# Kernel optimization log

Hardware: AMD Instinct MI355X
Metric: run time of the kernel (lower is better)

Reference implementation:

```python
import jax, jax.numpy as jnp
from jax import lax
import numpy as np

N_TOTAL = 262144
NUM_SAMPLE = 1024
KNN_K = 16
NUM_CLASSES = 13
HIDDEN = 128
EPS = 1e-8


def _sqdist(a, b):
    # (Na,3),(Nb,3) -> (Na,Nb) squared euclidean; same argmin as torch.cdist
    return (jnp.sum(a * a, axis=1)[:, None]
            + jnp.sum(b * b, axis=1)[None, :]
            - 2.0 * a @ b.T)


def _farthest_point_sample(xyz, n_samples):
    # sequential FPS starting from index 0 (deterministic start)
    n = xyz.shape[0]

    def step(carry, _):
        min_d2, last = carry
        d2 = jnp.sum((xyz - xyz[last]) ** 2, axis=-1)
        min_d2 = jnp.minimum(min_d2, d2)
        nxt = jnp.argmax(min_d2).astype(jnp.int32)
        return (min_d2, nxt), nxt

    init = (jnp.full((n,), 1e10, dtype=xyz.dtype), jnp.int32(0))
    _, idxs = lax.scan(step, init, None, length=n_samples - 1)
    return jnp.concatenate([jnp.zeros((1,), jnp.int32), idxs])


def _compute_normals(pts, k):
    # PCA normal per point from its k nearest neighbors (self excluded)
    d2 = _sqdist(pts, pts)                      # (S,S), S=1024 -> small
    _, nbr_idx = lax.top_k(-d2, k + 1)
    nbr = pts[nbr_idx[:, 1:]]                   # (S,k,3)
    centered = nbr - jnp.mean(nbr, axis=1, keepdims=True)
    cov = jnp.einsum('ski,skj->sij', centered, centered) / (k - 1)
    _, eigvecs = jnp.linalg.eigh(cov)           # ascending eigenvalues
    normal = eigvecs[..., 0]                    # smallest-eigval eigenvector
    return normal / (jnp.linalg.norm(normal, axis=-1, keepdims=True) + EPS)


def _forward(gaussian_positions, gaussian_colors, W1, b1, W2, b2, W3, b3):
    sample_idx = _farthest_point_sample(gaussian_positions, NUM_SAMPLE)
    dxyz = gaussian_positions[sample_idx]       # (S,3)
    drgb = gaussian_colors[sample_idx]          # (S,3)
    dnrm = _compute_normals(dxyz, KNN_K)        # (S,3)
    feats = jnp.concatenate([dxyz, drgb, dnrm], axis=1)  # (S,9)

    # pointwise segmentation network (stand-in for PointNet++ get_model)
    h = jax.nn.relu(feats @ W1 + b1)
    h = jax.nn.relu(h @ W2 + b2)
    pred = h @ W3 + b3                          # (S, num_classes)

    feat_down = jax.nn.softmax(pred, axis=1)
    lbl_down = jnp.argmax(pred, axis=1)

    # 1-NN label propagation: streaming-min candidate (memory-bound)
    d2_full = _sqdist(gaussian_positions, dxyz)  # (N, S) ~ 1 GB
    nearest = jnp.argmin(d2_full, axis=1)
    return feat_down[nearest], lbl_down[nearest]


def setup_inputs() -> dict:
    key = jax.random.key(0)
    ks = jax.random.split(key, 8)
    pos = jax.random.normal(ks[0], (N_TOTAL, 3), jnp.float32)
    col = jax.random.uniform(ks[1], (N_TOTAL, 3), jnp.float32)
    W1 = jax.random.normal(ks[2], (9, HIDDEN), jnp.float32) / np.sqrt(9.0)
    b1 = jnp.zeros((HIDDEN,), jnp.float32)
    W2 = jax.random.normal(ks[3], (HIDDEN, HIDDEN), jnp.float32) / np.sqrt(HIDDEN)
    b2 = jnp.zeros((HIDDEN,), jnp.float32)
    W3 = jax.random.normal(ks[4], (HIDDEN, NUM_CLASSES), jnp.float32) / np.sqrt(HIDDEN)
    b3 = jnp.zeros((NUM_CLASSES,), jnp.float32)
    return {"gaussian_positions": pos, "gaussian_colors": col,
            "W1": W1, "b1": b1, "W2": W2, "b2": b2, "W3": W3, "b3": b3}


def reference(gaussian_positions, gaussian_colors, W1, b1, W2, b2, W3, b3):
    return _forward(gaussian_positions, gaussian_colors, W1, b1, W2, b2, W3, b3)
```

## Files before the change

### kernel.cpp

```cpp
#include <hip/hip_runtime.h>
#include <math.h>

#define N_TOTAL    262144
#define NUM_SAMPLE 1024
#define FPS_BLOCKS 64
#define FPS_THREADS 256
#define FPS_PPT (N_TOTAL / (FPS_BLOCKS * FPS_THREADS))
#define M_WAVE 8
#define POOL (FPS_BLOCKS * 4 * M_WAVE)
#define ENT_PER_T (POOL / FPS_THREADS)
#define SEL_CAP 1023

__device__ __forceinline__ float addrn(float a, float b) { return __fadd_rn(a, b); }
__device__ __forceinline__ float subrn(float a, float b) { return __fsub_rn(a, b); }
__device__ __forceinline__ float mulrn(float a, float b) { return __fmul_rn(a, b); }

__device__ __forceinline__ float d2rn(float ax, float ay, float az,
                                      float bx, float by, float bz) {
  float dx = subrn(ax, bx), dy = subrn(ay, by), dz = subrn(az, bz);
  return addrn(addrn(mulrn(dx, dx), mulrn(dy, dy)), mulrn(dz, dz));
}

__device__ __forceinline__ unsigned long long shflxor_u64(unsigned long long v, int mk) {
  return (unsigned long long)__shfl_xor((long long)v, mk, 64);
}

template <int CTRL>
__device__ __forceinline__ int dpp_i(int x) {
  return __builtin_amdgcn_update_dpp(x, x, CTRL, 0xF, 0xF, false);
}
__device__ __forceinline__ float wave_fmax_bcast(float v) {
  v = fmaxf(v, __int_as_float(dpp_i<0x111>(__float_as_int(v))));
  v = fmaxf(v, __int_as_float(dpp_i<0x112>(__float_as_int(v))));
  v = fmaxf(v, __int_as_float(dpp_i<0x114>(__float_as_int(v))));
  v = fmaxf(v, __int_as_float(dpp_i<0x118>(__float_as_int(v))));
  v = fmaxf(v, __int_as_float(dpp_i<0x142>(__float_as_int(v))));
  v = fmaxf(v, __int_as_float(dpp_i<0x143>(__float_as_int(v))));
  return __int_as_float(__builtin_amdgcn_readlane(__float_as_int(v), 63));
}
__device__ __forceinline__ unsigned wave_umax_bcast(unsigned v) {
  unsigned o;
  o = (unsigned)dpp_i<0x111>((int)v); v = (o > v) ? o : v;
  o = (unsigned)dpp_i<0x112>((int)v); v = (o > v) ? o : v;
  o = (unsigned)dpp_i<0x114>((int)v); v = (o > v) ? o : v;
  o = (unsigned)dpp_i<0x118>((int)v); v = (o > v) ? o : v;
  o = (unsigned)dpp_i<0x142>((int)v); v = (o > v) ? o : v;
  o = (unsigned)dpp_i<0x143>((int)v); v = (o > v) ? o : v;
  return (unsigned)__builtin_amdgcn_readlane((int)v, 63);
}

__device__ __forceinline__ float slapy2f(float x, float y) {
  float xa = fabsf(x), ya = fabsf(y);
  float w = fmaxf(xa, ya), z = fminf(xa, ya);
  if (z == 0.f) return w;
  float t = z / w;
  return w * __fsqrt_rn(1.f + t * t);
}

__device__ __forceinline__ void slartgf(float f, float g, float& c, float& s, float& r) {
  if (g == 0.f) { c = 1.f; s = 0.f; r = f; }
  else if (f == 0.f) { c = 0.f; s = (g > 0.f) ? 1.f : -1.f; r = fabsf(g); }
  else {
    float d = __fsqrt_rn(f * f + g * g);
    c = fabsf(f) / d;
    r = (f >= 0.f) ? d : -d;
    s = g / r;
  }
}

__device__ void slaev2f(float a, float b, float c0, float& rt1, float& rt2,
                        float& cs1, float& sn1) {
  float sm = a + c0, df = a - c0;
  float adf = fabsf(df), tb = b + b, ab = fabsf(tb);
  float acmx, acmn;
  if (fabsf(a) > fabsf(c0)) { acmx = a; acmn = c0; } else { acmx = c0; acmn = a; }
  float rt;
  if (adf > ab)      { float t = ab / adf; rt = adf * __fsqrt_rn(1.f + t * t); }
  else if (adf < ab) { float t = adf / ab; rt = ab * __fsqrt_rn(1.f + t * t); }
  else               { rt = ab * __fsqrt_rn(2.f); }
  int sgn1;
  if (sm < 0.f)      { rt1 = 0.5f * (sm - rt); sgn1 = -1; rt2 = (acmx / rt1) * acmn - (b / rt1) * b; }
  else if (sm > 0.f) { rt1 = 0.5f * (sm + rt); sgn1 = 1;  rt2 = (acmx / rt1) * acmn - (b / rt1) * b; }
  else               { rt1 = 0.5f * rt; rt2 = -0.5f * rt; sgn1 = 1; }
  float cs; int sgn2;
  if (df >= 0.f) { cs = df + rt; sgn2 = 1; } else { cs = df - rt; sgn2 = -1; }
  float acs = fabsf(cs);
  if (acs > ab) {
    float ct = -tb / cs;
    sn1 = 1.f / __fsqrt_rn(1.f + ct * ct);
    cs1 = ct * sn1;
  } else {
    if (ab == 0.f) { cs1 = 1.f; sn1 = 0.f; }
    else { float tn = -cs / tb; cs1 = 1.f / __fsqrt_rn(1.f + tn * tn); sn1 = tn * cs1; }
  }
  if (sgn1 == sgn2) { float tn = cs1; cs1 = -sn1; sn1 = tn; }
}

#define D_(i) d[(i)-1]
#define E_(i) e[(i)-1]

__device__ void ssteqr3(float d[3], float e[2], float Z[3][3]) {
  const float eps    = 5.9604645e-08f;
  const float eps2   = 3.5527137e-15f;
  const float safmin = 1.17549435e-38f;
  const float ssfmax = 3.0744573e+18f;
  const float ssfmin = 3.0517578e-05f;
  const int n = 3;
  int jtot = 0, nmaxit = 90;
  int l1 = 1;

  while (true) {
    if (l1 > n) break;
    if (l1 > 1) E_(l1 - 1) = 0.f;
    int m = n;
    for (int mm = l1; mm <= n - 1; ++mm) {
      float tst = fabsf(E_(mm));
      if (tst == 0.f) { m = mm; break; }
      if (tst <= (__fsqrt_rn(fabsf(D_(mm))) * __fsqrt_rn(fabsf(D_(mm + 1)))) * eps) {
        E_(mm) = 0.f; m = mm; break;
      }
    }
    int l = l1, lsv = l, lend = m, lendsv = m;
    l1 = m + 1;
    if (lend == l) continue;

    float anorm = fabsf(D_(lend));
    for (int i2 = l; i2 <= lend - 1; ++i2) {
      anorm = fmaxf(anorm, fabsf(D_(i2)));
      anorm = fmaxf(anorm, fabsf(E_(i2)));
    }
    int iscale = 0;
    if (anorm == 0.f) continue;
    if (anorm > ssfmax) {
      iscale = 1; float mul = ssfmax / anorm;
      for (int i2 = l; i2 <= lend; ++i2) D_(i2) *= mul;
      for (int i2 = l; i2 <= lend - 1; ++i2) E_(i2) *= mul;
    } else if (anorm < ssfmin) {
      iscale = 2; float mul = ssfmin / anorm;
      for (int i2 = l; i2 <= lend; ++i2) D_(i2) *= mul;
      for (int i2 = l; i2 <= lend - 1; ++i2) E_(i2) *= mul;
    }

    if (fabsf(D_(lend)) < fabsf(D_(l))) { int t = l; l = lend; lend = t; }

    if (lend > l) {
      while (true) {
        int m2 = lend;
        if (l != lend) {
          for (int mm = l; mm <= lend - 1; ++mm) {
            float tst = fabsf(E_(mm)); tst = tst * tst;
            if (tst <= (eps2 * fabsf(D_(mm))) * fabsf(D_(mm + 1)) + safmin) { m2 = mm; break; }
          }
        }
        if (m2 < lend) E_(m2) = 0.f;
        float p = D_(l);
        if (m2 == l) { D_(l) = p; l = l + 1; if (l <= lend) continue; break; }
        if (m2 == l + 1) {
          float rt1, rt2, cc, ss;
          slaev2f(D_(l), E_(l), D_(l + 1), rt1, rt2, cc, ss);
          for (int i2 = 0; i2 < 3; ++i2) {
            float tmp = Z[i2][l];
            Z[i2][l]     = cc * tmp - ss * Z[i2][l - 1];
            Z[i2][l - 1] = ss * tmp + cc * Z[i2][l - 1];
          }
          D_(l) = rt1; D_(l + 1) = rt2; E_(l) = 0.f;
          l = l + 2; if (l <= lend) continue; break;
        }
        if (jtot == nmaxit) break;
        ++jtot;
        float g = (D_(l + 1) - p) / (2.f * E_(l));
        float r = slapy2f(g, 1.f);
        float sgn_rg = (g >= 0.f) ? r : -r;
        g = D_(m2) - p + E_(l) / (g + sgn_rg);
        float s = 1.f, c = 1.f;
        p = 0.f;
        float csv[2], ssv[2];
        for (int i2 = m2 - 1; i2 >= l; --i2) {
          float f = s * E_(i2);
          float b = c * E_(i2);
          slartgf(g, f, c, s, r);
          if (i2 != m2 - 1) E_(i2 + 1) = r;
          g = D_(i2 + 1) - p;
          r = (D_(i2) - g) * s + 2.f * c * b;
          p = s * r;
          D_(i2 + 1) = g + p;
          g = c * r - b;
          csv[i2 - l] = c; ssv[i2 - l] = -s;
        }
        for (int j = m2 - 1; j >= l; --j) {
          float ct = csv[j - l], st = ssv[j - l];
          for (int i2 = 0; i2 < 3; ++i2) {
            float tmp = Z[i2][j];
            Z[i2][j]     = ct * tmp - st * Z[i2][j - 1];
            Z[i2][j - 1] = st * tmp + ct * Z[i2][j - 1];
          }
        }
        D_(l) = D_(l) - p;
        E_(l) = g;
      }
    } else {
      while (true) {
        int m2 = lend;
        if (l != lend) {
          for (int mm = l; mm >= lend + 1; --mm) {
            float tst = fabsf(E_(mm - 1)); tst = tst * tst;
            if (tst <= (eps2 * fabsf(D_(mm))) * fabsf(D_(mm - 1)) + safmin) { m2 = mm; break; }
          }
        }
        if (m2 > lend) E_(m2 - 1) = 0.f;
        float p = D_(l);
        if (m2 == l) { D_(l) = p; l = l - 1; if (l >= lend) continue; break; }
        if (m2 == l - 1) {
          float rt1, rt2, cc, ss;
          slaev2f(D_(l - 1), E_(l - 1), D_(l), rt1, rt2, cc, ss);
          for (int i2 = 0; i2 < 3; ++i2) {
            float tmp = Z[i2][l - 1];
            Z[i2][l - 1] = cc * tmp - ss * Z[i2][l - 2];
            Z[i2][l - 2] = ss * tmp + cc * Z[i2][l - 2];
          }
          D_(l - 1) = rt1; D_(l) = rt2; E_(l - 1) = 0.f;
          l = l - 2; if (l >= lend) continue; break;
        }
        if (jtot == nmaxit) break;
        ++jtot;
        float g = (D_(l - 1) - p) / (2.f * E_(l - 1));
        float r = slapy2f(g, 1.f);
        float sgn_rg = (g >= 0.f) ? r : -r;
        g = D_(m2) - p + E_(l - 1) / (g + sgn_rg);
        float s = 1.f, c = 1.f;
        p = 0.f;
        float csv[2], ssv[2];
        for (int i2 = m2; i2 <= l - 1; ++i2) {
          float f = s * E_(i2);
          float b = c * E_(i2);
          slartgf(g, f, c, s, r);
          if (i2 != m2) E_(i2 - 1) = r;
          g = D_(i2) - p;
          r = (D_(i2 + 1) - g) * s + 2.f * c * b;
          p = s * r;
          D_(i2) = g + p;
          g = c * r - b;
          csv[i2 - m2] = c; ssv[i2 - m2] = s;
        }
        for (int j = m2; j <= l - 1; ++j) {
          float ct = csv[j - m2], st = ssv[j - m2];
          for (int i2 = 0; i2 < 3; ++i2) {
            float tmp = Z[i2][j];
            Z[i2][j]     = ct * tmp - st * Z[i2][j - 1];
            Z[i2][j - 1] = st * tmp + ct * Z[i2][j - 1];
          }
        }
        D_(l) = D_(l) - p;
        E_(l - 1) = g;
      }
    }
    if (iscale == 1) {
      float mul = anorm / ssfmax;
      for (int i2 = lsv; i2 <= lendsv; ++i2) D_(i2) *= mul;
      for (int i2 = lsv; i2 <= lendsv - 1; ++i2) E_(i2) *= mul;
    } else if (iscale == 2) {
      float mul = anorm / ssfmin;
      for (int i2 = lsv; i2 <= lendsv; ++i2) D_(i2) *= mul;
      for (int i2 = lsv; i2 <= lendsv - 1; ++i2) E_(i2) *= mul;
    }
  }
  for (int ii = 2; ii <= n; ++ii) {
    int i2 = ii - 1, k = i2;
    float p = D_(i2);
    for (int j = ii; j <= n; ++j) if (D_(j) < p) { k = j; p = D_(j); }
    if (k != i2) {
      D_(k) = D_(i2); D_(i2) = p;
      for (int rr = 0; rr < 3; ++rr) {
        float t = Z[rr][i2 - 1]; Z[rr][i2 - 1] = Z[rr][k - 1]; Z[rr][k - 1] = t;
      }
    }
  }
}

__device__ void eigh3_smallest(float a00, float a10, float a20, float a11, float a21, float a22,
                               float& nx, float& ny, float& nz) {
  float d[3], e[2];
  float Z[3][3] = {{1.f,0.f,0.f},{0.f,1.f,0.f},{0.f,0.f,1.f}};
  float tau, v2;
  {
    float alpha = a10, x = a20;
    float xnorm = fabsf(x);
    if (xnorm == 0.f) {
      tau = 0.f; v2 = 0.f;
      d[0] = a00; d[1] = a11; d[2] = a22;
      e[0] = alpha; e[1] = a21;
    } else {
      float beta = -copysignf(slapy2f(alpha, x), alpha);
      tau = (beta - alpha) / beta;
      v2 = x / (alpha - beta);
      float w0 = (tau * a11) + tau * (a21 * v2);
      float w1 = (tau * a21) + (tau * v2) * a22;
      float ac = (-0.5f * tau) * (w0 + w1 * v2);
      w0 = w0 + ac;
      w1 = w1 + ac * v2;
      d[0] = a00;
      d[1] = (a11 - w0) - w0;
      d[2] = (a22 - v2 * w1) - w1 * v2;
      e[0] = beta;
      e[1] = (a21 - v2 * w0) - w1;
    }
  }
  ssteqr3(d, e, Z);
  if (tau != 0.f) {
    for (int c = 0; c < 3; ++c) {
      float w = Z[1][c] + Z[2][c] * v2;
      float temp = (-tau) * w;
      Z[1][c] = Z[1][c] + temp;
      Z[2][c] = Z[2][c] + v2 * temp;
    }
  }
  nx = Z[0][0]; ny = Z[1][0]; nz = Z[2][0];
}

__global__ void k0_init(unsigned long long* cand, int* sample_idx) {
  int t = blockIdx.x * blockDim.x + threadIdx.x;
  if (t < 2 * POOL) cand[t] = 0ull;
  if (t == 0) sample_idx[0] = 0;
}

__global__ __launch_bounds__(FPS_THREADS) void k1_fps(
    const float* __restrict__ pos,
    unsigned long long* __restrict__ cand,
    int* __restrict__ sample_idx) {
  __shared__ float sel_x[SEL_CAP], sel_y[SEL_CAP], sel_z[SEL_CAP];
  __shared__ float wb_md[2][4], wb_x[2][4], wb_y[2][4], wb_z[2][4];
  __shared__ unsigned wb_idf[2][4];
  __shared__ float tred_md[4];
  __shared__ unsigned tred_idf[4];
  __shared__ int sh_selcnt;

  const int tidx = threadIdx.x;
  const int lane = tidx & 63, wv = tidx >> 6;
  const int gtid = blockIdx.x * FPS_THREADS + tidx;

  float px[FPS_PPT], py[FPS_PPT], pz[FPS_PPT], md[FPS_PPT];
#pragma unroll
  for (int k = 0; k < FPS_PPT; ++k) {
    int p = gtid + k * (FPS_BLOCKS * FPS_THREADS);
    px[k] = pos[3 * p]; py[k] = pos[3 * p + 1]; pz[k] = pos[3 * p + 2];
    md[k] = 1e10f;
  }
  const unsigned idf0 = 0x3FFFFFu - (unsigned)gtid;
  if (tidx == 0) { sel_x[0] = pos[0]; sel_y[0] = pos[1]; sel_z[0] = pos[2]; }
  __syncthreads();
  int sel_cnt = 1, total = 0, bt = 0;
  while (total < NUM_SAMPLE - 1) {
    ++bt;
    for (int s = 0; s < sel_cnt; ++s) {
      float lx = sel_x[s], ly = sel_y[s], lz = sel_z[s];
#pragma unroll
      for (int k = 0; k < FPS_PPT; ++k)
        md[k] = fminf(md[k], d2rn(px[k], py[k], pz[k], lx, ly, lz));
    }
    const unsigned tag = (unsigned)bt & 1023u;
    unsigned long long* setbase = cand + (size_t)(bt & 1) * POOL;
    {
      float wmd[FPS_PPT];
#pragma unroll
      for (int k = 0; k < FPS_PPT; ++k) wmd[k] = md[k];
      unsigned long long mypub = 0ull;
      for (int r = 0; r < M_WAVE; ++r) {
        float bm = wmd[0]; unsigned bidf = idf0;
#pragma unroll
        for (int k = 1; k < FPS_PPT; ++k) {
          unsigned idfk = idf0 - ((unsigned)k << 14);
          if (wmd[k] > bm || (wmd[k] == bm && idfk > bidf)) { bm = wmd[k]; bidf = idfk; }
        }
        float wmx = wave_fmax_bcast(bm);
        unsigned tb = (bm == wmx) ? bidf : 0u;
        unsigned widf = wave_umax_bcast(tb);
        if (lane == r)
          mypub = ((unsigned long long)__float_as_uint(wmx) << 32) |
                  ((unsigned long long)widf << 10);
#pragma unroll
        for (int k = 0; k < FPS_PPT; ++k) {
          unsigned idfk = idf0 - ((unsigned)k << 14);
          if (wmd[k] == wmx && idfk == widf) wmd[k] = -1.f;
        }
      }
      if (lane < M_WAVE)
        __hip_atomic_store(setbase + blockIdx.x * (4 * M_WAVE) + wv * M_WAVE + lane,
                           mypub | tag, __ATOMIC_RELAXED, __HIP_MEMORY_SCOPE_AGENT);
    }
    const int base_w = tidx * ENT_PER_T;
    float cmd[ENT_PER_T]; unsigned cidf[ENT_PER_T];
    {
      unsigned done = 0;
      while (done != 0xFFu) {
#pragma unroll
        for (int j = 0; j < ENT_PER_T; ++j) {
          if (!((done >> j) & 1u)) {
            unsigned long long v = __hip_atomic_load(setbase + base_w + j,
                                                     __ATOMIC_RELAXED, __HIP_MEMORY_SCOPE_AGENT);
            if ((unsigned)(v & 1023ull) == tag) {
              done |= 1u << j;
              cmd[j] = __uint_as_float((unsigned)(v >> 32));
              cidf[j] = (unsigned)((v >> 10) & 0x3FFFFFull);
            }
          }
        }
        if (done != 0xFFu) __builtin_amdgcn_s_sleep(1);
      }
    }
    float cx[ENT_PER_T], cy[ENT_PER_T], cz[ENT_PER_T];
#pragma unroll
    for (int j = 0; j < ENT_PER_T; ++j) {
      int gidx = 0x3FFFFF - (int)cidf[j];
      cx[j] = pos[3 * gidx]; cy[j] = pos[3 * gidx + 1]; cz[j] = pos[3 * gidx + 2];
    }
    {
      float t7 = cmd[ENT_PER_T - 1]; unsigned t7i = cidf[ENT_PER_T - 1];
      float twm = wave_fmax_bcast(t7);
      unsigned ttb = (t7 == twm) ? t7i : 0u;
      unsigned twi = wave_umax_bcast(ttb);
      if (lane == 0) { tred_md[wv] = twm; tred_idf[wv] = twi; }
    }
    __syncthreads();
    float Tmd = tred_md[0]; unsigned Tidf = tred_idf[0];
#pragma unroll
    for (int w = 1; w < 4; ++w) {
      float m2 = tred_md[w]; unsigned i2v = tred_idf[w];
      if (m2 > Tmd || (m2 == Tmd && i2v > Tidf)) { Tmd = m2; Tidf = i2v; }
    }
    int picks = 0;
    const int room = (NUM_SAMPLE - 1) - total;
    for (;;) {
      const int q = picks & 1;
      float bm = cmd[0]; unsigned bidf = cidf[0]; int bj = 0;
#pragma unroll
      for (int j = 1; j < ENT_PER_T; ++j)
        if (cmd[j] > bm || (cmd[j] == bm && cidf[j] > bidf)) { bm = cmd[j]; bidf = cidf[j]; bj = j; }
      float wmx = wave_fmax_bcast(bm);
      unsigned tb = (bm == wmx) ? bidf : 0u;
      unsigned widf = wave_umax_bcast(tb);
      if (bm == wmx && bidf == widf) {
        wb_md[q][wv] = wmx; wb_idf[q][wv] = widf;
        wb_x[q][wv] = cx[bj]; wb_y[q][wv] = cy[bj]; wb_z[q][wv] = cz[bj];
      }
      __syncthreads();
      float gm = wb_md[q][0]; unsigned gi = wb_idf[q][0]; int gw = 0;
#pragma unroll
      for (int w = 1; w < 4; ++w) {
        float m2 = wb_md[q][w]; unsigned i2v = wb_idf[q][w];
        if (m2 > gm || (m2 == gm && i2v > gi)) { gm = m2; gi = i2v; gw = w; }
      }
      if ((gm < Tmd || (gm == Tmd && gi < Tidf)) || picks >= room) break;
      float Xp = wb_x[q][gw], Yp = wb_y[q][gw], Zp = wb_z[q][gw];
      if (tidx == 0) {
        sel_x[picks] = Xp; sel_y[picks] = Yp; sel_z[picks] = Zp;
        if (blockIdx.x == 0) sample_idx[1 + total + picks] = 0x3FFFFF - (int)gi;
      }
#pragma unroll
      for (int j = 0; j < ENT_PER_T; ++j) {
        if (cmd[j] == gm && cidf[j] == gi) cmd[j] = -1.f;
        float d2 = d2rn(cx[j], cy[j], cz[j], Xp, Yp, Zp);
        if (d2 < cmd[j]) cmd[j] = d2;
      }
      ++picks;
    }
    if (tidx == 0) sh_selcnt = picks;
    __syncthreads();
    sel_cnt = sh_selcnt;
    total += sel_cnt;
  }
}

__global__ __launch_bounds__(256) void k2a_knn(
    const float* __restrict__ pos, const float* __restrict__ col,
    const int* __restrict__ sample_idx,
    float4* __restrict__ sp4g, float* __restrict__ feats9) {
  __shared__ float4 sp[NUM_SAMPLE];
  const int tid = threadIdx.x, lane = tid & 63, wv = tid >> 6;
  for (int i = tid; i < NUM_SAMPLE; i += 256) {
    int idx = sample_idx[i];
    float x = pos[3 * idx], y = pos[3 * idx + 1], z = pos[3 * idx + 2];
    float nrm = addrn(addrn(mulrn(x, x), mulrn(y, y)), mulrn(z, z));
    float4 v = make_float4(x, y, z, nrm);
    sp[i] = v;
    if (blockIdx.x == 0) sp4g[i] = v;
  }
  __syncthreads();
  for (int it = 0; it < 4; ++it) {
    const int r = blockIdx.x * 16 + wv * 4 + it;
    float4 pr = sp[r];
    unsigned long long kk[16];
#pragma unroll
    for (int k = 0; k < 16; ++k) {
      int j = lane + 64 * k;
      float4 q = sp[j];
      float dot = fmaf(pr.z, q.z, fmaf(pr.y, q.y, mulrn(pr.x, q.x)));
      float d2 = subrn(addrn(pr.w, q.w), mulrn(2.f, dot));
      unsigned b = __float_as_uint(d2);
      unsigned sbits = (b & 0x80000000u) ? ~b : (b | 0x80000000u);
      kk[k] = ((unsigned long long)sbits << 32) | (unsigned)j;
    }
    int bi[17];
#pragma unroll
    for (int rsel = 0; rsel < 17; ++rsel) {
      unsigned long long best = 0xFFFFFFFFFFFFFFFFull;
#pragma unroll
      for (int k = 0; k < 16; ++k) best = (kk[k] < best) ? kk[k] : best;
#pragma unroll
      for (int mk = 1; mk < 64; mk <<= 1) {
        unsigned long long o = (unsigned long long)__shfl_xor((long long)best, mk, 64);
        best = (o < best) ? o : best;
      }
      int j = (int)(best & 0xFFFFFFFFull);
      bi[rsel] = j;
#pragma unroll
      for (int k = 0; k < 16; ++k)
        if (((j >> 6) == k) && ((j & 63) == lane)) kk[k] = 0xFFFFFFFFFFFFFFFFull;
    }
    float mx = 0.f, my = 0.f, mz = 0.f;
#pragma unroll
    for (int k = 1; k <= 16; ++k) {
      float4 q = sp[bi[k]];
      mx = addrn(mx, q.x); my = addrn(my, q.y); mz = addrn(mz, q.z);
    }
    mx = mulrn(mx, 0.0625f); my = mulrn(my, 0.0625f); mz = mulrn(mz, 0.0625f);
    float c00 = 0.f, c01 = 0.f, c02 = 0.f, c11 = 0.f, c12 = 0.f, c22 = 0.f;
#pragma unroll
    for (int k = 1; k <= 16; ++k) {
      float4 q = sp[bi[k]];
      float dx = subrn(q.x, mx), dy = subrn(q.y, my), dz = subrn(q.z, mz);
      c00 = addrn(c00, mulrn(dx, dx)); c01 = addrn(c01, mulrn(dx, dy));
      c02 = addrn(c02, mulrn(dx, dz)); c11 = addrn(c11, mulrn(dy, dy));
      c12 = addrn(c12, mulrn(dy, dz)); c22 = addrn(c22, mulrn(dz, dz));
    }
    c00 /= 15.f; c01 /= 15.f; c02 /= 15.f; c11 /= 15.f; c12 /= 15.f; c22 /= 15.f;

    float n0, n1, n2;
    eigh3_smallest(c00, c01, c02, c11, c12, c22, n0, n1, n2);
    float nn = __fsqrt_rn(addrn(addrn(mulrn(n0, n0), mulrn(n1, n1)), mulrn(n2, n2)));
    float den = addrn(nn, 1e-8f);
    n0 /= den; n1 /= den; n2 /= den;

    if (lane == 0) {
      int myidx = sample_idx[r];
      float* f = feats9 + r * 9;
      f[0] = pr.x; f[1] = pr.y; f[2] = pr.z;
      f[3] = col[3 * myidx]; f[4] = col[3 * myidx + 1]; f[5] = col[3 * myidx + 2];
      f[6] = n0; f[7] = n1; f[8] = n2;
    }
  }
}

__global__ __launch_bounds__(64) void k2b_mlp(
    const float* __restrict__ W1, const float* __restrict__ b1,
    const float* __restrict__ W2, const float* __restrict__ b2,
    const float* __restrict__ W3, const float* __restrict__ b3,
    const float* __restrict__ feats9,
    float* __restrict__ featd, int* __restrict__ lbl) {
  __shared__ float hbuf[64][129];
  const int tid = threadIdx.x;
  const int r = blockIdx.x * 64 + tid;
  float f9[9];
#pragma unroll
  for (int k = 0; k < 9; ++k) f9[k] = feats9[r * 9 + k];
  for (int jo = 0; jo < 128; ++jo) {
    float acc = 0.f;
#pragma unroll
    for (int k = 0; k < 9; ++k) acc = fmaf(f9[k], W1[k * 128 + jo], acc);
    acc += b1[jo];
    hbuf[tid][jo] = fmaxf(acc, 0.f);
  }
  float pd[13];
#pragma unroll
  for (int c = 0; c < 13; ++c) pd[c] = 0.f;
  for (int io = 0; io < 128; io += 16) {
    float acc[16];
#pragma unroll
    for (int t = 0; t < 16; ++t) acc[t] = 0.f;
    for (int j = 0; j < 128; ++j) {
      float hj = hbuf[tid][j];
#pragma unroll
      for (int t = 0; t < 16; ++t) acc[t] = fmaf(hj, W2[j * 128 + io + t], acc[t]);
    }
#pragma unroll
    for (int t = 0; t < 16; ++t) {
      float h2 = fmaxf(acc[t] + b2[io + t], 0.f);
#pragma unroll
      for (int c = 0; c < 13; ++c) pd[c] = fmaf(h2, W3[(io + t) * 13 + c], pd[c]);
    }
  }
#pragma unroll
  for (int c = 0; c < 13; ++c) pd[c] += b3[c];
  float mmax = pd[0];
#pragma unroll
  for (int c = 1; c < 13; ++c) mmax = fmaxf(mmax, pd[c]);
  float es = 0.f, ev[13];
#pragma unroll
  for (int c = 0; c < 13; ++c) { ev[c] = expf(pd[c] - mmax); es += ev[c]; }
#pragma unroll
  for (int c = 0; c < 13; ++c) featd[r * 13 + c] = ev[c] / es;
  int am = 0; float bv = pd[0];
#pragma unroll
  for (int c = 1; c < 13; ++c) { if (pd[c] > bv) { bv = pd[c]; am = c; } }
  lbl[r] = am;
}

__global__ __launch_bounds__(256) void k3_assign(
    const float* __restrict__ pos,
    const float4* __restrict__ sp4g,
    const float* __restrict__ featd,
    const int* __restrict__ lbl,
    float* __restrict__ out) {
  __shared__ float4 sp[NUM_SAMPLE];
  for (int i = threadIdx.x; i < NUM_SAMPLE; i += 256) sp[i] = sp4g[i];
  __syncthreads();
  int i = blockIdx.x * 256 + threadIdx.x;
  float x = pos[3 * i], y = pos[3 * i + 1], z = pos[3 * i + 2];
  float an = addrn(addrn(mulrn(x, x), mulrn(y, y)), mulrn(z, z));
  float bestd = 3.402823466e+38f; int bestj = 0;
#pragma unroll 4
  for (int j = 0; j < NUM_SAMPLE; ++j) {
    float4 q = sp[j];
    float dot = fmaf(z, q.z, fmaf(y, q.y, mulrn(x, q.x)));
    float d2 = subrn(addrn(an, q.w), mulrn(2.f, dot));
    if (d2 < bestd) { bestd = d2; bestj = j; }
  }
  const float* fr = featd + bestj * 13;
  float* o = out + (size_t)i * 13;
#pragma unroll
  for (int c = 0; c < 13; ++c) o[c] = fr[c];
  out[(size_t)N_TOTAL * 13 + i] = (float)lbl[bestj];
}

extern "C" void kernel_launch(void* const* d_in, const int* in_sizes, int n_in,
                              void* d_out, int out_size, void* d_ws, size_t ws_size,
                              hipStream_t stream) {
  (void)in_sizes; (void)n_in; (void)out_size; (void)ws_size;
  const float* pos = (const float*)d_in[0];
  const float* col = (const float*)d_in[1];
  const float* W1 = (const float*)d_in[2];
  const float* b1 = (const float*)d_in[3];
  const float* W2 = (const float*)d_in[4];
  const float* b2 = (const float*)d_in[5];
  const float* W3 = (const float*)d_in[6];
  const float* b3 = (const float*)d_in[7];
  float* out = (float*)d_out;

  char* w = (char*)d_ws;
  unsigned long long* cand = (unsigned long long*)(w);
  int* sample_idx = (int*)(w + 65536);
  float4* sp4g = (float4*)(w + 73728);
  float* featd = (float*)(w + 90112);
  int* lbl = (int*)(w + 143360);
  float* feats9 = (float*)(w + 147456);

  k0_init<<<16, 256, 0, stream>>>(cand, sample_idx);
  k1_fps<<<FPS_BLOCKS, FPS_THREADS, 0, stream>>>(pos, cand, sample_idx);
  k2a_knn<<<64, 256, 0, stream>>>(pos, col, sample_idx, sp4g, feats9);
  k2b_mlp<<<16, 64, 0, stream>>>(W1, b1, W2, b2, W3, b3, feats9, featd, lbl);
  k3_assign<<<N_TOTAL / 256, 256, 0, stream>>>(pos, sp4g, featd, lbl, out);
}
```

Baseline: 1.926 ms.

## Run FPS candidate selection in a single wave with a top-2 active set

The per-pick candidate selection inside each FPS batch is restructured. Previously all four waves took part in every pick and synchronized through shared memory with __syncthreads. Now each thread keeps its top-2 candidates in an active set of 512 entries that one wave selects from, with no block barriers between picks. A per-thread third-best threshold decides when that set has to be refilled from the full per-thread lists. Candidate position loads are also moved into the polling loop so they overlap with waiting. This is meant to cut barrier and cross-wave reduction latency on the serial critical path, at the cost of more shared memory, more complex refill logic, and exact tie-break semantics that must be kept.

```diff
diff --git a/kernel.cpp b/kernel.cpp
--- a/kernel.cpp
+++ b/kernel.cpp
@@ -9,6 +9,7 @@
 #define M_WAVE 8
 #define POOL (FPS_BLOCKS * 4 * M_WAVE)
 #define ENT_PER_T (POOL / FPS_THREADS)
+#define ACT 512
 #define SEL_CAP 1023
 
 __device__ __forceinline__ float addrn(float a, float b) { return __fadd_rn(a, b); }
@@ -21,8 +22,11 @@
   return addrn(addrn(mulrn(dx, dx), mulrn(dy, dy)), mulrn(dz, dz));
 }
 
-__device__ __forceinline__ unsigned long long shflxor_u64(unsigned long long v, int mk) {
-  return (unsigned long long)__shfl_xor((long long)v, mk, 64);
+__device__ __forceinline__ bool lex_gt(float m1, unsigned i1, float m2, unsigned i2) {
+  return (m1 > m2) || (m1 == m2 && i1 > i2);
+}
+__device__ __forceinline__ bool lex_ge(float m1, unsigned i1, float m2, unsigned i2) {
+  return (m1 > m2) || (m1 == m2 && i1 >= i2);
 }
 
 template <int CTRL>
@@ -328,11 +332,15 @@
     unsigned long long* __restrict__ cand,
     int* __restrict__ sample_idx) {
   __shared__ float sel_x[SEL_CAP], sel_y[SEL_CAP], sel_z[SEL_CAP];
-  __shared__ float wb_md[2][4], wb_x[2][4], wb_y[2][4], wb_z[2][4];
-  __shared__ unsigned wb_idf[2][4];
   __shared__ float tred_md[4];
   __shared__ unsigned tred_idf[4];
-  __shared__ int sh_selcnt;
+  __shared__ float t2red_md[4];
+  __shared__ unsigned t2red_idf[4];
+  __shared__ float act_md[ACT], act_x[ACT], act_y[ACT], act_z[ACT];
+  __shared__ unsigned act_idf[ACT];
+  __shared__ float thr3_md[FPS_THREADS];
+  __shared__ unsigned thr3_idf[FPS_THREADS];
+  __shared__ int sh_flag, sh_pc;
 
   const int tidx = threadIdx.x;
   const int lane = tidx & 63, wv = tidx >> 6;
@@ -389,6 +397,7 @@
     }
     const int base_w = tidx * ENT_PER_T;
     float cmd[ENT_PER_T]; unsigned cidf[ENT_PER_T];
+    float cx[ENT_PER_T], cy[ENT_PER_T], cz[ENT_PER_T];
     {
       unsigned done = 0;
       while (done != 0xFFu) {
@@ -401,72 +410,152 @@
               done |= 1u << j;
               cmd[j] = __uint_as_float((unsigned)(v >> 32));
               cidf[j] = (unsigned)((v >> 10) & 0x3FFFFFull);
+              int gidx = 0x3FFFFF - (int)cidf[j];
+              cx[j] = pos[3 * gidx]; cy[j] = pos[3 * gidx + 1]; cz[j] = pos[3 * gidx + 2];
             }
           }
         }
         if (done != 0xFFu) __builtin_amdgcn_s_sleep(1);
       }
-    }
-    float cx[ENT_PER_T], cy[ENT_PER_T], cz[ENT_PER_T];
-#pragma unroll
-    for (int j = 0; j < ENT_PER_T; ++j) {
-      int gidx = 0x3FFFFF - (int)cidf[j];
-      cx[j] = pos[3 * gidx]; cy[j] = pos[3 * gidx + 1]; cz[j] = pos[3 * gidx + 2];
     }
     {
       float t7 = cmd[ENT_PER_T - 1]; unsigned t7i = cidf[ENT_PER_T - 1];
-      float twm = wave_fmax_bcast(t7);
-      unsigned ttb = (t7 == twm) ? t7i : 0u;
-      unsigned twi = wave_umax_bcast(ttb);
-      if (lane == 0) { tred_md[wv] = twm; tred_idf[wv] = twi; }
+      float w7 = wave_fmax_bcast(t7);
+      unsigned tb7 = (t7 == w7) ? t7i : 0u;
+      unsigned w7i = wave_umax_bcast(tb7);
+      if (lane == 0) { tred_md[wv] = w7; tred_idf[wv] = w7i; }
+      float t2 = cmd[2]; unsigned t2i = cidf[2];
+      float w2 = wave_fmax_bcast(t2);
+      unsigned tb2 = (t2 == w2) ? t2i : 0u;
+      unsigned w2i = wave_umax_bcast(tb2);
+      if (lane == 0) { t2red_md[wv] = w2; t2red_idf[wv] = w2i; }
+      int e = 2 * tidx;
+      act_md[e] = cmd[0]; act_idf[e] = cidf[0];
+      act_x[e] = cx[0]; act_y[e] = cy[0]; act_z[e] = cz[0];
+      act_md[e + 1] = cmd[1]; act_idf[e + 1] = cidf[1];
+      act_x[e + 1] = cx[1]; act_y[e + 1] = cy[1]; act_z[e + 1] = cz[1];
     }
     __syncthreads();
     float Tmd = tred_md[0]; unsigned Tidf = tred_idf[0];
+    float T2m = t2red_md[0]; unsigned T2i = t2red_idf[0];
 #pragma unroll
     for (int w = 1; w < 4; ++w) {
-      float m2 = tred_md[w]; unsigned i2v = tred_idf[w];
-      if (m2 > Tmd || (m2 == Tmd && i2v > Tidf)) { Tmd = m2; Tidf = i2v; }
-    }
-    int picks = 0;
+      if (lex_gt(tred_md[w], tred_idf[w], Tmd, Tidf)) { Tmd = tred_md[w]; Tidf = tred_idf[w]; }
+      if (lex_gt(t2red_md[w], t2red_idf[w], T2m, T2i)) { T2m = t2red_md[w]; T2i = t2red_idf[w]; }
+    }
     const int room = (NUM_SAMPLE - 1) - total;
+    float q_md[8], q_x[8], q_y[8], q_z[8];
+    unsigned q_idf[8];
+    if (tidx < 64) {
+#pragma unroll
+      for (int r = 0; r < 8; ++r) {
+        int e2 = lane + 64 * r;
+        q_md[r] = act_md[e2]; q_idf[r] = act_idf[e2];
+        q_x[r] = act_x[e2]; q_y[r] = act_y[e2]; q_z[r] = act_z[e2];
+      }
+    }
+    int picks = 0, myq = 0, pc = 0;
     for (;;) {
-      const int q = picks & 1;
-      float bm = cmd[0]; unsigned bidf = cidf[0]; int bj = 0;
-#pragma unroll
-      for (int j = 1; j < ENT_PER_T; ++j)
-        if (cmd[j] > bm || (cmd[j] == bm && cidf[j] > bidf)) { bm = cmd[j]; bidf = cidf[j]; bj = j; }
-      float wmx = wave_fmax_bcast(bm);
-      unsigned tb = (bm == wmx) ? bidf : 0u;
-      unsigned widf = wave_umax_bcast(tb);
-      if (bm == wmx && bidf == widf) {
-        wb_md[q][wv] = wmx; wb_idf[q][wv] = widf;
-        wb_x[q][wv] = cx[bj]; wb_y[q][wv] = cy[bj]; wb_z[q][wv] = cz[bj];
+      if (tidx < 64) {
+        int ev = 0;
+        for (;;) {
+          float bm = q_md[0]; unsigned bidf = q_idf[0];
+          float bx = q_x[0], by = q_y[0], bz = q_z[0];
+#pragma unroll
+          for (int j = 1; j < 8; ++j) {
+            bool g = (q_md[j] > bm) || (q_md[j] == bm && q_idf[j] > bidf);
+            if (g) { bm = q_md[j]; bidf = q_idf[j]; bx = q_x[j]; by = q_y[j]; bz = q_z[j]; }
+          }
+          float wmx = wave_fmax_bcast(bm);
+          unsigned long long ball = __ballot(bm == wmx);
+          unsigned widf; int owner;
+          if (__builtin_popcountll(ball) == 1) {
+            owner = __builtin_ctzll(ball);
+            widf = (unsigned)__builtin_amdgcn_readlane((int)bidf, owner);
+          } else {
+            unsigned tb = (bm == wmx) ? bidf : 0u;
+            widf = wave_umax_bcast(tb);
+            owner = __builtin_ctzll(__ballot(bm == wmx && bidf == widf));
+          }
+          if (picks >= room) { ev = 0; break; }
+          if (!lex_ge(wmx, widf, T2m, T2i)) { ev = 1; break; }
+          if (!lex_ge(wmx, widf, Tmd, Tidf)) { ev = 0; break; }
+          float X = __int_as_float(__builtin_amdgcn_readlane(__float_as_int(bx), owner));
+          float Y = __int_as_float(__builtin_amdgcn_readlane(__float_as_int(by), owner));
+          float Z = __int_as_float(__builtin_amdgcn_readlane(__float_as_int(bz), owner));
+          if (lane == 0) {
+            sel_x[picks] = X; sel_y[picks] = Y; sel_z[picks] = Z;
+            if (blockIdx.x == 0) sample_idx[1 + total + picks] = 0x3FFFFF - (int)widf;
+          }
+#pragma unroll
+          for (int j = 0; j < 8; ++j)
+            q_md[j] = fminf(q_md[j], d2rn(q_x[j], q_y[j], q_z[j], X, Y, Z));
+          ++picks;
+        }
+        if (lane == 0) { sh_flag = ev; sh_pc = picks; }
       }
       __syncthreads();
-      float gm = wb_md[q][0]; unsigned gi = wb_idf[q][0]; int gw = 0;
-#pragma unroll
-      for (int w = 1; w < 4; ++w) {
-        float m2 = wb_md[q][w]; unsigned i2v = wb_idf[q][w];
-        if (m2 > gm || (m2 == gm && i2v > gi)) { gm = m2; gi = i2v; gw = w; }
-      }
-      if ((gm < Tmd || (gm == Tmd && gi < Tidf)) || picks >= room) break;
-      float Xp = wb_x[q][gw], Yp = wb_y[q][gw], Zp = wb_z[q][gw];
-      if (tidx == 0) {
-        sel_x[picks] = Xp; sel_y[picks] = Yp; sel_z[picks] = Zp;
-        if (blockIdx.x == 0) sample_idx[1 + total + picks] = 0x3FFFFF - (int)gi;
-      }
-#pragma unroll
-      for (int j = 0; j < ENT_PER_T; ++j) {
-        if (cmd[j] == gm && cidf[j] == gi) cmd[j] = -1.f;
-        float d2 = d2rn(cx[j], cy[j], cz[j], Xp, Yp, Zp);
-        if (d2 < cmd[j]) cmd[j] = d2;
-      }
-      ++picks;
-    }
-    if (tidx == 0) sh_selcnt = picks;
-    __syncthreads();
-    sel_cnt = sh_selcnt;
-    total += sel_cnt;
+      int ev = sh_flag; pc = sh_pc;
+      if (ev == 0) break;
+      for (int q = myq; q < pc; ++q) {
+        float lx = sel_x[q], ly = sel_y[q], lz = sel_z[q];
+#pragma unroll
+        for (int j = 0; j < ENT_PER_T; ++j)
+          cmd[j] = fminf(cmd[j], d2rn(cx[j], cy[j], cz[j], lx, ly, lz));
+      }
+      myq = pc;
+      {
+        float m1 = -1.f, m2 = -1.f, m3 = -1.f;
+        unsigned i1 = 0u, i2v = 0u, i3v = 0u;
+        float x1 = 0.f, y1 = 0.f, z1 = 0.f, x2 = 0.f, y2 = 0.f, z2 = 0.f;
+#pragma unroll
+        for (int j = 0; j < ENT_PER_T; ++j) {
+          float m = cmd[j]; unsigned ii = cidf[j];
+          float xx = cx[j], yy = cy[j], zz = cz[j];
+          bool g1 = lex_gt(m, ii, m1, i1);
+          bool g2 = lex_gt(m, ii, m2, i2v);
+          bool g3 = lex_gt(m, ii, m3, i3v);
+          float nm3 = g2 ? m2 : (g3 ? m : m3); unsigned ni3 = g2 ? i2v : (g3 ? ii : i3v);
+          float nm2 = g1 ? m1 : (g2 ? m : m2); unsigned ni2 = g1 ? i1 : (g2 ? ii : i2v);
+          float nx2 = g1 ? x1 : (g2 ? xx : x2);
+          float ny2 = g1 ? y1 : (g2 ? yy : y2);
+          float nz2 = g1 ? z1 : (g2 ? zz : z2);
+          float nm1 = g1 ? m : m1; unsigned ni1 = g1 ? ii : i1;
+          float nx1 = g1 ? xx : x1;
+          float ny1 = g1 ? yy : y1;
+          float nz1 = g1 ? zz : z1;
+          m3 = nm3; i3v = ni3;
+          m2 = nm2; i2v = ni2; x2 = nx2; y2 = ny2; z2 = nz2;
+          m1 = nm1; i1 = ni1; x1 = nx1; y1 = ny1; z1 = nz1;
+        }
+        int e = 2 * tidx;
+        act_md[e] = m1; act_idf[e] = i1; act_x[e] = x1; act_y[e] = y1; act_z[e] = z1;
+        act_md[e + 1] = m2; act_idf[e + 1] = i2v;
+        act_x[e + 1] = x2; act_y[e + 1] = y2; act_z[e + 1] = z2;
+        thr3_md[tidx] = m3; thr3_idf[tidx] = i3v;
+      }
+      __syncthreads();
+      if (tidx < 64) {
+#pragma unroll
+        for (int r = 0; r < 8; ++r) {
+          int e2 = lane + 64 * r;
+          q_md[r] = act_md[e2]; q_idf[r] = act_idf[e2];
+          q_x[r] = act_x[e2]; q_y[r] = act_y[e2]; q_z[r] = act_z[e2];
+        }
+        float rm = thr3_md[lane]; unsigned ri = thr3_idf[lane];
+#pragma unroll
+        for (int r = 1; r < 4; ++r) {
+          float m = thr3_md[lane + 64 * r]; unsigned ii = thr3_idf[lane + 64 * r];
+          if (lex_gt(m, ii, rm, ri)) { rm = m; ri = ii; }
+        }
+        float wm = wave_fmax_bcast(rm);
+        unsigned tb = (rm == wm) ? ri : 0u;
+        unsigned wi = wave_umax_bcast(tb);
+        T2m = wm; T2i = wi;
+      }
+    }
+    sel_cnt = pc;
+    total += pc;
   }
 }
 
```

Result: faster. 1.827 ms (-5.1%).

## Run FPS candidate pick loop in a single wave without block barriers

Applied to the files above, without the earlier changes.

The per-round greedy pick loop now runs in one 64-lane wave. Candidates are staged into shared memory and each lane holds POOL/64 entries, so the per-pick __syncthreads across four waves goes away. A ballot fast path finds the argmax owner without a second reduction. Candidate position loads now happen while the poll loop runs, and the selected-point reads are software-prefetched as float4. The other three waves sit idle during the pick phase, and each lane now holds more entries to scan per pick.

```diff
diff --git a/kernel.cpp b/kernel.cpp
--- a/kernel.cpp
+++ b/kernel.cpp
@@ -9,6 +9,7 @@
 #define M_WAVE 8
 #define POOL (FPS_BLOCKS * 4 * M_WAVE)
 #define ENT_PER_T (POOL / FPS_THREADS)
+#define QD (POOL / 64)
 #define SEL_CAP 1023
 
 __device__ __forceinline__ float addrn(float a, float b) { return __fadd_rn(a, b); }
@@ -21,8 +22,11 @@
   return addrn(addrn(mulrn(dx, dx), mulrn(dy, dy)), mulrn(dz, dz));
 }
 
-__device__ __forceinline__ unsigned long long shflxor_u64(unsigned long long v, int mk) {
-  return (unsigned long long)__shfl_xor((long long)v, mk, 64);
+__device__ __forceinline__ bool lex_gt(float m1, unsigned i1, float m2, unsigned i2) {
+  return (m1 > m2) || (m1 == m2 && i1 > i2);
+}
+__device__ __forceinline__ bool lex_ge(float m1, unsigned i1, float m2, unsigned i2) {
+  return (m1 > m2) || (m1 == m2 && i1 >= i2);
 }
 
 template <int CTRL>
@@ -323,19 +327,19 @@
   if (t == 0) sample_idx[0] = 0;
 }
 
-__global__ __launch_bounds__(FPS_THREADS) void k1_fps(
+__global__ __launch_bounds__(FPS_THREADS, 1) void k1_fps(
     const float* __restrict__ pos,
     unsigned long long* __restrict__ cand,
     int* __restrict__ sample_idx) {
-  __shared__ float sel_x[SEL_CAP], sel_y[SEL_CAP], sel_z[SEL_CAP];
-  __shared__ float wb_md[2][4], wb_x[2][4], wb_y[2][4], wb_z[2][4];
-  __shared__ unsigned wb_idf[2][4];
-  __shared__ float tred_md[4];
-  __shared__ unsigned tred_idf[4];
-  __shared__ int sh_selcnt;
+  __shared__ float4 sel4[SEL_CAP];
+  __shared__ float4 act4[POOL];
+  __shared__ unsigned act_idf[POOL];
+  __shared__ float thrT_md[FPS_THREADS];
+  __shared__ unsigned thrT_idf[FPS_THREADS];
+  __shared__ int sh_pc;
 
   const int tidx = threadIdx.x;
-  const int lane = tidx & 63, wv = tidx >> 6;
+  const int lane = tidx & 63;
   const int gtid = blockIdx.x * FPS_THREADS + tidx;
 
   float px[FPS_PPT], py[FPS_PPT], pz[FPS_PPT], md[FPS_PPT];
@@ -346,20 +350,25 @@
     md[k] = 1e10f;
   }
   const unsigned idf0 = 0x3FFFFFu - (unsigned)gtid;
-  if (tidx == 0) { sel_x[0] = pos[0]; sel_y[0] = pos[1]; sel_z[0] = pos[2]; }
+  if (tidx == 0) sel4[0] = make_float4(pos[0], pos[1], pos[2], 0.f);
   __syncthreads();
   int sel_cnt = 1, total = 0, bt = 0;
   while (total < NUM_SAMPLE - 1) {
     ++bt;
-    for (int s = 0; s < sel_cnt; ++s) {
-      float lx = sel_x[s], ly = sel_y[s], lz = sel_z[s];
-#pragma unroll
-      for (int k = 0; k < FPS_PPT; ++k)
-        md[k] = fminf(md[k], d2rn(px[k], py[k], pz[k], lx, ly, lz));
+    {
+      float4 sc = sel4[0];
+      for (int s = 0; s < sel_cnt; ++s) {
+        float4 sn = (s + 1 < sel_cnt) ? sel4[s + 1] : sc;
+#pragma unroll
+        for (int k = 0; k < FPS_PPT; ++k)
+          md[k] = fminf(md[k], d2rn(px[k], py[k], pz[k], sc.x, sc.y, sc.z));
+        sc = sn;
+      }
     }
     const unsigned tag = (unsigned)bt & 1023u;
     unsigned long long* setbase = cand + (size_t)(bt & 1) * POOL;
     {
+      const int wv = tidx >> 6;
       float wmd[FPS_PPT];
 #pragma unroll
       for (int k = 0; k < FPS_PPT; ++k) wmd[k] = md[k];
@@ -384,12 +393,13 @@
         }
       }
       if (lane < M_WAVE)
-        __hip_atomic_store(setbase + blockIdx.x * (4 * M_WAVE) + wv * M_WAVE + lane,
+        __hip_atomic_store(setbase + blockIdx.x * (4 * M_WAVE) + (tidx >> 6) * M_WAVE + lane,
                            mypub | tag, __ATOMIC_RELAXED, __HIP_MEMORY_SCOPE_AGENT);
     }
     const int base_w = tidx * ENT_PER_T;
-    float cmd[ENT_PER_T]; unsigned cidf[ENT_PER_T];
     {
+      float cmd[ENT_PER_T]; unsigned cidf[ENT_PER_T];
+      float cx[ENT_PER_T], cy[ENT_PER_T], cz[ENT_PER_T];
       unsigned done = 0;
       while (done != 0xFFu) {
 #pragma unroll
@@ -401,71 +411,79 @@
               done |= 1u << j;
               cmd[j] = __uint_as_float((unsigned)(v >> 32));
               cidf[j] = (unsigned)((v >> 10) & 0x3FFFFFull);
+              int gidx = 0x3FFFFF - (int)cidf[j];
+              cx[j] = pos[3 * gidx]; cy[j] = pos[3 * gidx + 1]; cz[j] = pos[3 * gidx + 2];
             }
           }
         }
         if (done != 0xFFu) __builtin_amdgcn_s_sleep(1);
       }
-    }
-    float cx[ENT_PER_T], cy[ENT_PER_T], cz[ENT_PER_T];
-#pragma unroll
-    for (int j = 0; j < ENT_PER_T; ++j) {
-      int gidx = 0x3FFFFF - (int)cidf[j];
-      cx[j] = pos[3 * gidx]; cy[j] = pos[3 * gidx + 1]; cz[j] = pos[3 * gidx + 2];
-    }
-    {
-      float t7 = cmd[ENT_PER_T - 1]; unsigned t7i = cidf[ENT_PER_T - 1];
-      float twm = wave_fmax_bcast(t7);
-      unsigned ttb = (t7 == twm) ? t7i : 0u;
-      unsigned twi = wave_umax_bcast(ttb);
-      if (lane == 0) { tred_md[wv] = twm; tred_idf[wv] = twi; }
+#pragma unroll
+      for (int j = 0; j < ENT_PER_T; ++j) {
+        int e = tidx * ENT_PER_T + j;
+        act4[e] = make_float4(cx[j], cy[j], cz[j], cmd[j]);
+        act_idf[e] = cidf[j];
+      }
+      thrT_md[tidx] = cmd[ENT_PER_T - 1]; thrT_idf[tidx] = cidf[ENT_PER_T - 1];
     }
     __syncthreads();
-    float Tmd = tred_md[0]; unsigned Tidf = tred_idf[0];
-#pragma unroll
-    for (int w = 1; w < 4; ++w) {
-      float m2 = tred_md[w]; unsigned i2v = tred_idf[w];
-      if (m2 > Tmd || (m2 == Tmd && i2v > Tidf)) { Tmd = m2; Tidf = i2v; }
-    }
-    int picks = 0;
     const int room = (NUM_SAMPLE - 1) - total;
-    for (;;) {
-      const int q = picks & 1;
-      float bm = cmd[0]; unsigned bidf = cidf[0]; int bj = 0;
-#pragma unroll
-      for (int j = 1; j < ENT_PER_T; ++j)
-        if (cmd[j] > bm || (cmd[j] == bm && cidf[j] > bidf)) { bm = cmd[j]; bidf = cidf[j]; bj = j; }
-      float wmx = wave_fmax_bcast(bm);
-      unsigned tb = (bm == wmx) ? bidf : 0u;
-      unsigned widf = wave_umax_bcast(tb);
-      if (bm == wmx && bidf == widf) {
-        wb_md[q][wv] = wmx; wb_idf[q][wv] = widf;
-        wb_x[q][wv] = cx[bj]; wb_y[q][wv] = cy[bj]; wb_z[q][wv] = cz[bj];
-      }
-      __syncthreads();
-      float gm = wb_md[q][0]; unsigned gi = wb_idf[q][0]; int gw = 0;
-#pragma unroll
-      for (int w = 1; w < 4; ++w) {
-        float m2 = wb_md[q][w]; unsigned i2v = wb_idf[q][w];
-        if (m2 > gm || (m2 == gm && i2v > gi)) { gm = m2; gi = i2v; gw = w; }
-      }
-      if ((gm < Tmd || (gm == Tmd && gi < Tidf)) || picks >= room) break;
-      float Xp = wb_x[q][gw], Yp = wb_y[q][gw], Zp = wb_z[q][gw];
-      if (tidx == 0) {
-        sel_x[picks] = Xp; sel_y[picks] = Yp; sel_z[picks] = Zp;
-        if (blockIdx.x == 0) sample_idx[1 + total + picks] = 0x3FFFFF - (int)gi;
-      }
-#pragma unroll
-      for (int j = 0; j < ENT_PER_T; ++j) {
-        if (cmd[j] == gm && cidf[j] == gi) cmd[j] = -1.f;
-        float d2 = d2rn(cx[j], cy[j], cz[j], Xp, Yp, Zp);
-        if (d2 < cmd[j]) cmd[j] = d2;
-      }
-      ++picks;
-    }
-    if (tidx == 0) sh_selcnt = picks;
+    if (tidx < 64) {
+      float q_md[QD], q_x[QD], q_y[QD], q_z[QD];
+      unsigned q_idf[QD];
+#pragma unroll
+      for (int r = 0; r < QD; ++r) {
+        int e2 = lane + 64 * r;
+        float4 a = act4[e2];
+        q_x[r] = a.x; q_y[r] = a.y; q_z[r] = a.z; q_md[r] = a.w;
+        q_idf[r] = act_idf[e2];
+      }
+      float rm = thrT_md[lane]; unsigned ri = thrT_idf[lane];
+#pragma unroll
+      for (int r = 1; r < 4; ++r) {
+        float m = thrT_md[lane + 64 * r]; unsigned ii = thrT_idf[lane + 64 * r];
+        if (lex_gt(m, ii, rm, ri)) { rm = m; ri = ii; }
+      }
+      float Tmd = wave_fmax_bcast(rm);
+      unsigned tbT = (rm == Tmd) ? ri : 0u;
+      unsigned Tidf = wave_umax_bcast(tbT);
+
+      int picks = 0;
+      float X = 1e30f, Y = 1e30f, Z = 1e30f;
+      for (;;) {
+        float bm = -1.f; unsigned bidf = 0u; int bj = 0;
+#pragma unroll
+        for (int j = 0; j < QD; ++j) {
+          float nd = fminf(q_md[j], d2rn(q_x[j], q_y[j], q_z[j], X, Y, Z));
+          q_md[j] = nd;
+          if (lex_gt(nd, q_idf[j], bm, bidf)) { bm = nd; bidf = q_idf[j]; bj = j; }
+        }
+        float wmx = wave_fmax_bcast(bm);
+        unsigned long long ball = __ballot(bm == wmx);
+        unsigned widf; int owner;
+        if (__builtin_popcountll(ball) == 1) {
+          owner = __builtin_ctzll(ball);
+          widf = (unsigned)__builtin_amdgcn_readlane((int)bidf, owner);
+        } else {
+          unsigned tb = (bm == wmx) ? bidf : 0u;
+          widf = wave_umax_bcast(tb);
+          owner = __builtin_ctzll(__ballot(bm == wmx && bidf == widf));
+        }
+        if (picks >= room) break;
+        if (!lex_ge(wmx, widf, Tmd, Tidf)) break;
+        int bjo = __builtin_amdgcn_readlane(bj, owner);
+        float4 wc = act4[owner + 64 * bjo];
+        X = wc.x; Y = wc.y; Z = wc.z;
+        if (lane == 0) {
+          sel4[picks] = make_float4(X, Y, Z, 0.f);
+          if (blockIdx.x == 0) sample_idx[1 + total + picks] = 0x3FFFFF - (int)widf;
+        }
+        ++picks;
+      }
+      if (lane == 0) sh_pc = picks;
+    }
     __syncthreads();
-    sel_cnt = sh_selcnt;
+    sel_cnt = sh_pc;
     total += sel_cnt;
   }
 }
```

Result: slower. 2.327 ms (+20.8%).
